# Kernel tuning notes

Measured on AMD Instinct MI355X. Metric: run time of the kernel, lower is better.

The kernel has to match this reference:

```python
import jax, jax.numpy as jnp
import numpy as np

B, S, D = 8, 2048, 512

def setup_inputs() -> dict:
    key = jax.random.key(0)
    k1, k2, k3 = jax.random.split(key, 3)
    context = jax.random.normal(k1, (B, S, D), dtype=jnp.float32)
    # nn.Linear default init ~ U(-1/sqrt(D), 1/sqrt(D)); scale keeps softmax sane
    bound = 1.0 / np.sqrt(D)
    W_in = jax.random.uniform(k2, (D, D), dtype=jnp.float32, minval=-bound, maxval=bound)
    W_out = jax.random.uniform(k3, (D, D), dtype=jnp.float32, minval=-bound, maxval=bound)
    return {"context": context, "W_in": W_in, "W_out": W_out}

def reference(context, W_in, W_out):
    # linear_in: x @ W_in.T (torch Linear convention)
    c = jnp.einsum('bsd,ed->bse', context, W_in)            # [B,S,D]
    scores = jnp.einsum('bsd,btd->bst', c, c)               # [B,S,S], no 1/sqrt(d) scale
    attn = jax.nn.softmax(scores, axis=-1)                  # [B,S,S]
    ctx = jnp.einsum('bst,btd->bsd', attn, c)               # [B,S,D]
    out = jnp.einsum('bsd,ed->bse', jnp.tanh(ctx), W_out)   # linear_out
    return out, attn
```

## Files before the change

kernel.cpp:

```cpp
#include <hip/hip_runtime.h>
#include <cstdint>
#include <cstddef>

#define Bc 8
#define Sc 2048
#define Dc 512

typedef float f32x4 __attribute__((ext_vector_type(4)));
typedef __bf16 bf16x8 __attribute__((ext_vector_type(8)));
typedef __bf16 bf16x4 __attribute__((ext_vector_type(4)));

__device__ __forceinline__ void gload_lds16(const void* g, void* l) {
    __builtin_amdgcn_global_load_lds((const __attribute__((address_space(1))) void*)g,
                                     (__attribute__((address_space(3))) void*)l, 16, 0, 0);
}

__device__ __forceinline__ f32x4 mfma16x16x32(bf16x8 a, bf16x8 b, f32x4 c) {
    return __builtin_amdgcn_mfma_f32_16x16x32_bf16(a, b, c, 0, 0, 0);
}

__global__ void k_convert_w(const float* __restrict__ wi, const float* __restrict__ wo,
                            __bf16* __restrict__ wib, __bf16* __restrict__ wob) {
    int i = blockIdx.x * 256 + threadIdx.x;
    wib[i] = (__bf16)wi[i];
    wob[i] = (__bf16)wo[i];
}

template <bool STATS>
__global__ __launch_bounds__(256) void k_gemm_bf16(
        const __bf16* __restrict__ A, const __bf16* __restrict__ Bt,
        float* __restrict__ C, float2* __restrict__ stats,
        int lda, int ldb, int ldc, int K,
        size_t aOffZ, size_t bOffZ, size_t cOffZ)
{
    __shared__ alignas(16) __bf16 smem[2 * 128 * 64];
    __bf16* As = smem;
    __bf16* Bs = smem + 128 * 64;
    const int tid  = threadIdx.x;
    const int wave = tid >> 6, lane = tid & 63;
    const int waveM = wave >> 1, waveN = wave & 1;
    int row0, col0, bz;
    if constexpr (STATS) {
        const int bid = blockIdx.x;
        bz   = bid & 7;
        col0 = ((bid >> 3) & 15) * 128;
        row0 = (bid >> 7) * 128;
    } else {
        bz = blockIdx.z; row0 = blockIdx.y * 128; col0 = blockIdx.x * 128;
    }
    A  += (size_t)bz * aOffZ;
    Bt += (size_t)bz * bOffZ;
    C  += (size_t)bz * cOffZ;

    f32x4 acc[4][4] = {};

    for (int k0 = 0; k0 < K; k0 += 64) {
        #pragma unroll
        for (int i = 0; i < 4; ++i) {
            int flat = i * 2048 + wave * 512 + lane * 8;
            int r  = flat >> 6;
            int cc = (flat >> 3) & 7;
            int gc = (cc ^ (r & 7)) << 3;
            gload_lds16(A  + (size_t)(row0 + r) * lda + k0 + gc, As + i * 2048 + wave * 512);
            gload_lds16(Bt + (size_t)(col0 + r) * ldb + k0 + gc, Bs + i * 2048 + wave * 512);
        }
        __syncthreads();
        #pragma unroll
        for (int ks = 0; ks < 2; ++ks) {
            const int kc = ks * 4 + (lane >> 4);
            bf16x8 av[4], bv[4];
            #pragma unroll
            for (int mi = 0; mi < 4; ++mi) {
                int r = waveM * 64 + mi * 16 + (lane & 15);
                av[mi] = *(const bf16x8*)&As[r * 64 + ((kc ^ (r & 7)) << 3)];
            }
            #pragma unroll
            for (int ni = 0; ni < 4; ++ni) {
                int r = waveN * 64 + ni * 16 + (lane & 15);
                bv[ni] = *(const bf16x8*)&Bs[r * 64 + ((kc ^ (r & 7)) << 3)];
            }
            #pragma unroll
            for (int mi = 0; mi < 4; ++mi)
                #pragma unroll
                for (int ni = 0; ni < 4; ++ni)
                    acc[mi][ni] = mfma16x16x32(av[mi], bv[ni], acc[mi][ni]);
        }
        __syncthreads();
    }

    const int rb = (lane >> 4) << 2;
    const int cb = lane & 15;
    #pragma unroll
    for (int mi = 0; mi < 4; ++mi)
        #pragma unroll
        for (int ni = 0; ni < 4; ++ni) {
            int gr = row0 + waveM * 64 + mi * 16 + rb;
            int gc = col0 + waveN * 64 + ni * 16 + cb;
            #pragma unroll
            for (int rr = 0; rr < 4; ++rr)
                C[(size_t)(gr + rr) * ldc + gc] = acc[mi][ni][rr];
        }

    if constexpr (STATS) {
        float2* sm = (float2*)smem;
        #pragma unroll
        for (int mi = 0; mi < 4; ++mi)
            #pragma unroll
            for (int rr = 0; rr < 4; ++rr) {
                float mx = fmaxf(fmaxf(acc[mi][0][rr], acc[mi][1][rr]),
                                 fmaxf(acc[mi][2][rr], acc[mi][3][rr]));
                #pragma unroll
                for (int off = 1; off < 16; off <<= 1) mx = fmaxf(mx, __shfl_xor(mx, off));
                float zs = 0.f;
                #pragma unroll
                for (int ni = 0; ni < 4; ++ni) zs += __expf(acc[mi][ni][rr] - mx);
                #pragma unroll
                for (int off = 1; off < 16; off <<= 1) zs += __shfl_xor(zs, off);
                if ((lane & 15) == 0)
                    sm[waveN * 128 + waveM * 64 + mi * 16 + rb + rr] = make_float2(mx, zs);
            }
        __syncthreads();
        if (tid < 128) {
            float2 a2 = sm[tid], b2 = sm[128 + tid];
            float M = fmaxf(a2.x, b2.x);
            float Z = a2.y * __expf(a2.x - M) + b2.y * __expf(b2.x - M);
            stats[((size_t)bz * Sc + row0 + tid) * 16 + (col0 >> 7)] = make_float2(M, Z);
        }
    }
}

__global__ __launch_bounds__(256) void k_stat_combine(const float2* __restrict__ stats,
                                                      float2* __restrict__ rowstat) {
    int r = blockIdx.x * 256 + threadIdx.x;
    float2 s[16];
    #pragma unroll
    for (int i = 0; i < 16; ++i) s[i] = stats[(size_t)r * 16 + i];
    float M = s[0].x;
    #pragma unroll
    for (int i = 1; i < 16; ++i) M = fmaxf(M, s[i].x);
    float Z = 0.f;
    #pragma unroll
    for (int i = 0; i < 16; ++i) Z += s[i].y * __expf(s[i].x - M);
    rowstat[r] = make_float2(M, 1.f / Z);
}

__global__ __launch_bounds__(512) void k_pv_fused(
        float* __restrict__ attn,
        const __bf16* __restrict__ cT,
        const float2* __restrict__ rowstat,
        __bf16* __restrict__ ctx)
{
    __shared__ alignas(16) __bf16 As[2][64 * 32];
    __shared__ alignas(16) __bf16 Bs[2][512 * 32];
    const int tid  = threadIdx.x;
    const int wave = tid >> 6, lane = tid & 63;
    const int b    = blockIdx.x & 7;
    const int row0 = (blockIdx.x >> 3) * 64;
    float* sc = attn + (size_t)b * Sc * Sc;
    const __bf16* Bt = cT + (size_t)b * Dc * Sc;

    const int ar = tid >> 3;
    const int ac = (tid & 7) * 4;
    const float2 st = rowstat[b * Sc + row0 + ar];
    const float m_row = st.x, zinv = st.y;
    const int a_addr = ar * 32 + (((ac >> 3) ^ (ar & 3)) << 3) + (ac & 7);
    float* srow = sc + (size_t)(row0 + ar) * Sc + ac;

    f32x4 acc[4][4] = {};

    auto stageB = [&](int buf, int kt) {
        #pragma unroll
        for (int i = 0; i < 4; ++i) {
            int chunk = i * 512 + wave * 64 + lane;
            int r  = chunk >> 2;
            int cc = chunk & 3;
            gload_lds16(Bt + (size_t)r * Sc + kt + ((cc ^ (r & 3)) << 3),
                        &Bs[buf][(i * 512 + wave * 64) * 8]);
        }
    };

    const int NT = Sc / 32;

    f32x4 s_next = *(const f32x4*)&srow[0];
    f32x4 p;
    #pragma unroll
    for (int j = 0; j < 4; ++j) p[j] = __expf(s_next[j] - m_row) * zinv;
    {
        bf16x4 pb;
        #pragma unroll
        for (int j = 0; j < 4; ++j) pb[j] = (__bf16)p[j];
        *(bf16x4*)&As[0][a_addr] = pb;
    }
    stageB(0, 0);
    s_next = *(const f32x4*)&srow[32];
    __syncthreads();

    for (int t = 0; t < NT; ++t) {
        const int cur = t & 1;
        if (t + 1 < NT) {
            f32x4 pn;
            #pragma unroll
            for (int j = 0; j < 4; ++j) pn[j] = __expf(s_next[j] - m_row) * zinv;
            bf16x4 pb;
            #pragma unroll
            for (int j = 0; j < 4; ++j) pb[j] = (__bf16)pn[j];
            *(bf16x4*)&As[cur ^ 1][a_addr] = pb;
            stageB(cur ^ 1, (t + 1) * 32);
            *(f32x4*)&srow[t * 32] = p;
            if (t + 2 < NT) s_next = *(const f32x4*)&srow[(t + 2) * 32];
            p = pn;
        } else {
            *(f32x4*)&srow[t * 32] = p;
        }
        const int kc = lane >> 4;
        bf16x8 av[4], bv[4];
        #pragma unroll
        for (int mi = 0; mi < 4; ++mi) {
            int r = mi * 16 + (lane & 15);
            av[mi] = *(const bf16x8*)&As[cur][r * 32 + ((kc ^ (r & 3)) << 3)];
        }
        #pragma unroll
        for (int ni = 0; ni < 4; ++ni) {
            int r = wave * 64 + ni * 16 + (lane & 15);
            bv[ni] = *(const bf16x8*)&Bs[cur][r * 32 + ((kc ^ (r & 3)) << 3)];
        }
        #pragma unroll
        for (int mi = 0; mi < 4; ++mi)
            #pragma unroll
            for (int ni = 0; ni < 4; ++ni)
                acc[mi][ni] = mfma16x16x32(av[mi], bv[ni], acc[mi][ni]);
        __syncthreads();
    }

    const int rb = (lane >> 4) << 2;
    const int cb = lane & 15;
    #pragma unroll
    for (int mi = 0; mi < 4; ++mi)
        #pragma unroll
        for (int ni = 0; ni < 4; ++ni) {
            int gr = row0 + mi * 16 + rb;
            int gc = wave * 64 + ni * 16 + cb;
            #pragma unroll
            for (int rr = 0; rr < 4; ++rr)
                ctx[(size_t)(b * Sc + gr + rr) * Dc + gc] = (__bf16)tanhf(acc[mi][ni][rr]);
        }
}

__global__ __launch_bounds__(256) void k_cproj(
        const float* __restrict__ A, const __bf16* __restrict__ Bt,
        __bf16* __restrict__ Cb, __bf16* __restrict__ CTb)
{
    __shared__ alignas(16) char smem[49152];
    float*  Asf = (float*)smem;
    __bf16* Bs  = (__bf16*)(smem + 32768);
    const int tid  = threadIdx.x;
    const int wave = tid >> 6, lane = tid & 63;
    const int waveM = wave >> 1, waveN = wave & 1;
    const int row0 = blockIdx.y * 128;
    const int col0 = blockIdx.x * 128;

    f32x4 acc[4][4] = {};

    for (int k0 = 0; k0 < Dc; k0 += 64) {
        #pragma unroll
        for (int i = 0; i < 8; ++i) {
            int flat = i * 1024 + wave * 256 + lane * 4;
            int r  = flat >> 6;
            int cc = (flat >> 2) & 15;
            int gc = (cc ^ (r & 15)) << 2;
            gload_lds16(A + (size_t)(row0 + r) * Dc + k0 + gc, Asf + i * 1024 + wave * 256);
        }
        #pragma unroll
        for (int i = 0; i < 4; ++i) {
            int flat = i * 2048 + wave * 512 + lane * 8;
            int r  = flat >> 6;
            int cc = (flat >> 3) & 7;
            int gc = (cc ^ (r & 7)) << 3;
            gload_lds16(Bt + (size_t)(col0 + r) * Dc + k0 + gc, Bs + i * 2048 + wave * 512);
        }
        __syncthreads();
        #pragma unroll
        for (int ks = 0; ks < 2; ++ks) {
            const int kc8 = ks * 4 + (lane >> 4);
            const int kc4 = kc8 << 1;
            bf16x8 av[4], bv[4];
            #pragma unroll
            for (int mi = 0; mi < 4; ++mi) {
                int r  = waveM * 64 + mi * 16 + (lane & 15);
                int r4 = r & 15;
                f32x4 lo = *(const f32x4*)&Asf[r * 64 + (((kc4    ) ^ r4) << 2)];
                f32x4 hi = *(const f32x4*)&Asf[r * 64 + (((kc4 + 1) ^ r4) << 2)];
                bf16x8 a;
                a[0] = (__bf16)lo[0]; a[1] = (__bf16)lo[1]; a[2] = (__bf16)lo[2]; a[3] = (__bf16)lo[3];
                a[4] = (__bf16)hi[0]; a[5] = (__bf16)hi[1]; a[6] = (__bf16)hi[2]; a[7] = (__bf16)hi[3];
                av[mi] = a;
            }
            #pragma unroll
            for (int ni = 0; ni < 4; ++ni) {
                int r = waveN * 64 + ni * 16 + (lane & 15);
                bv[ni] = *(const bf16x8*)&Bs[r * 64 + ((kc8 ^ (r & 7)) << 3)];
            }
            #pragma unroll
            for (int mi = 0; mi < 4; ++mi)
                #pragma unroll
                for (int ni = 0; ni < 4; ++ni)
                    acc[mi][ni] = mfma16x16x32(av[mi], bv[ni], acc[mi][ni]);
        }
        __syncthreads();
    }

    const int rb = (lane >> 4) << 2;
    const int cb = lane & 15;
    __bf16* T = (__bf16*)smem;
    #pragma unroll
    for (int mi = 0; mi < 4; ++mi)
        #pragma unroll
        for (int ni = 0; ni < 4; ++ni) {
            int lr = waveM * 64 + mi * 16 + rb;
            int lc = waveN * 64 + ni * 16 + cb;
            #pragma unroll
            for (int rr = 0; rr < 4; ++rr) {
                __bf16 h = (__bf16)acc[mi][ni][rr];
                Cb[(size_t)(row0 + lr + rr) * Dc + col0 + lc] = h;
                T[lc * 136 + lr + rr] = h;
            }
        }
    __syncthreads();
    const int bb = row0 >> 11;
    const int s0 = row0 & 2047;
    #pragma unroll
    for (int i = 0; i < 8; ++i) {
        int n  = i * 16 + (tid >> 4);
        int mo = (tid & 15) * 8;
        bf16x8 v = *(const bf16x8*)&T[n * 136 + mo];
        *(bf16x8*)&CTb[(size_t)bb * Dc * Sc + (size_t)(col0 + n) * Sc + s0 + mo] = v;
    }
}

extern "C" void kernel_launch(void* const* d_in, const int* in_sizes, int n_in,
                              void* d_out, int out_size, void* d_ws, size_t ws_size,
                              hipStream_t stream)
{
    (void)in_sizes; (void)n_in; (void)out_size; (void)ws_size;
    const float* context = (const float*)d_in[0];
    const float* W_in    = (const float*)d_in[1];
    const float* W_out   = (const float*)d_in[2];
    float* out  = (float*)d_out;
    float* attn = out + (size_t)Bc * Sc * Dc;

    char* ws = (char*)d_ws;
    __bf16* c_bf    = (__bf16*)ws;
    __bf16* cT_bf   = (__bf16*)(ws + 16777216);
    __bf16* wi_bf   = (__bf16*)(ws + 33554432);
    __bf16* wo_bf   = (__bf16*)(ws + 34078720);
    float2* stats   = (float2*)(ws + 34603008);
    float2* rowstat = (float2*)(ws + 36700160);

    k_convert_w<<<dim3(Dc * Dc / 256), 256, 0, stream>>>(W_in, W_out, wi_bf, wo_bf);

    k_cproj<<<dim3(Dc / 128, (Bc * Sc) / 128), 256, 0, stream>>>(context, wi_bf, c_bf, cT_bf);

    k_gemm_bf16<true><<<dim3(Bc * 16 * 16), 256, 0, stream>>>(
        c_bf, c_bf, attn, stats, Dc, Dc, Sc, Dc,
        (size_t)Sc * Dc, (size_t)Sc * Dc, (size_t)Sc * Sc);

    k_stat_combine<<<dim3(Bc * Sc / 256), 256, 0, stream>>>(stats, rowstat);

    k_pv_fused<<<dim3((Sc / 64) * Bc), 512, 0, stream>>>(attn, cT_bf, rowstat, c_bf);

    k_gemm_bf16<false><<<dim3(Dc / 128, (Bc * Sc) / 128, 1), 256, 0, stream>>>(
        c_bf, wo_bf, out, nullptr, Dc, Dc, Dc, Dc, 0, 0, 0);
}
```

Before: 201.3 us.

## Load B operand directly from global in PV kernel, single-buffer A with 64-wide K

```diff
diff --git a/kernel.cpp b/kernel.cpp
--- a/kernel.cpp
+++ b/kernel.cpp
@@ -150,8 +150,7 @@
         const float2* __restrict__ rowstat,
         __bf16* __restrict__ ctx)
 {
-    __shared__ alignas(16) __bf16 As[2][64 * 32];
-    __shared__ alignas(16) __bf16 Bs[2][512 * 32];
+    __shared__ alignas(16) __bf16 As[64 * 64];
     const int tid  = threadIdx.x;
     const int wave = tid >> 6, lane = tid & 63;
     const int b    = blockIdx.x & 7;
@@ -160,76 +159,88 @@
     const __bf16* Bt = cT + (size_t)b * Dc * Sc;
 
     const int ar = tid >> 3;
-    const int ac = (tid & 7) * 4;
+    const int ac = (tid & 7) * 8;
     const float2 st = rowstat[b * Sc + row0 + ar];
     const float m_row = st.x, zinv = st.y;
-    const int a_addr = ar * 32 + (((ac >> 3) ^ (ar & 3)) << 3) + (ac & 7);
+    const int a_addr = ar * 64 + ((((ac >> 3)) ^ (ar & 7)) << 3);
     float* srow = sc + (size_t)(row0 + ar) * Sc + ac;
 
+    const __bf16* bbase[4];
+    #pragma unroll
+    for (int ni = 0; ni < 4; ++ni)
+        bbase[ni] = Bt + (size_t)(wave * 64 + ni * 16 + (lane & 15)) * Sc + (lane >> 4) * 8;
+
     f32x4 acc[4][4] = {};
 
-    auto stageB = [&](int buf, int kt) {
-        #pragma unroll
-        for (int i = 0; i < 4; ++i) {
-            int chunk = i * 512 + wave * 64 + lane;
-            int r  = chunk >> 2;
-            int cc = chunk & 3;
-            gload_lds16(Bt + (size_t)r * Sc + kt + ((cc ^ (r & 3)) << 3),
-                        &Bs[buf][(i * 512 + wave * 64) * 8]);
-        }
-    };
-
-    const int NT = Sc / 32;
-
-    f32x4 s_next = *(const f32x4*)&srow[0];
-    f32x4 p;
-    #pragma unroll
-    for (int j = 0; j < 4; ++j) p[j] = __expf(s_next[j] - m_row) * zinv;
+    const int NT = Sc / 64;
+
+    f32x4 sn0 = *(const f32x4*)&srow[0];
+    f32x4 sn1 = *(const f32x4*)&srow[4];
     {
-        bf16x4 pb;
-        #pragma unroll
-        for (int j = 0; j < 4; ++j) pb[j] = (__bf16)p[j];
-        *(bf16x4*)&As[0][a_addr] = pb;
-    }
-    stageB(0, 0);
-    s_next = *(const f32x4*)&srow[32];
-    __syncthreads();
+        f32x4 p0, p1;
+        #pragma unroll
+        for (int j = 0; j < 4; ++j) {
+            p0[j] = __expf(sn0[j] - m_row) * zinv;
+            p1[j] = __expf(sn1[j] - m_row) * zinv;
+        }
+        bf16x8 pb;
+        #pragma unroll
+        for (int j = 0; j < 4; ++j) { pb[j] = (__bf16)p0[j]; pb[4 + j] = (__bf16)p1[j]; }
+        *(bf16x8*)&As[a_addr] = pb;
+        *(f32x4*)&srow[0] = p0;
+        *(f32x4*)&srow[4] = p1;
+    }
+    asm volatile("s_waitcnt lgkmcnt(0)" ::: "memory");
+    __builtin_amdgcn_s_barrier();
+    sn0 = *(const f32x4*)&srow[64];
+    sn1 = *(const f32x4*)&srow[68];
 
     for (int t = 0; t < NT; ++t) {
-        const int cur = t & 1;
+        bf16x8 av[4][2];
+        #pragma unroll
+        for (int ks = 0; ks < 2; ++ks) {
+            const int kc = ks * 4 + (lane >> 4);
+            #pragma unroll
+            for (int mi = 0; mi < 4; ++mi) {
+                int r = mi * 16 + (lane & 15);
+                av[mi][ks] = *(const bf16x8*)&As[r * 64 + ((kc ^ (r & 7)) << 3)];
+            }
+        }
+        __builtin_amdgcn_s_barrier();
         if (t + 1 < NT) {
-            f32x4 pn;
-            #pragma unroll
-            for (int j = 0; j < 4; ++j) pn[j] = __expf(s_next[j] - m_row) * zinv;
-            bf16x4 pb;
-            #pragma unroll
-            for (int j = 0; j < 4; ++j) pb[j] = (__bf16)pn[j];
-            *(bf16x4*)&As[cur ^ 1][a_addr] = pb;
-            stageB(cur ^ 1, (t + 1) * 32);
-            *(f32x4*)&srow[t * 32] = p;
-            if (t + 2 < NT) s_next = *(const f32x4*)&srow[(t + 2) * 32];
-            p = pn;
-        } else {
-            *(f32x4*)&srow[t * 32] = p;
-        }
-        const int kc = lane >> 4;
-        bf16x8 av[4], bv[4];
-        #pragma unroll
-        for (int mi = 0; mi < 4; ++mi) {
-            int r = mi * 16 + (lane & 15);
-            av[mi] = *(const bf16x8*)&As[cur][r * 32 + ((kc ^ (r & 3)) << 3)];
-        }
-        #pragma unroll
-        for (int ni = 0; ni < 4; ++ni) {
-            int r = wave * 64 + ni * 16 + (lane & 15);
-            bv[ni] = *(const bf16x8*)&Bs[cur][r * 32 + ((kc ^ (r & 3)) << 3)];
-        }
-        #pragma unroll
-        for (int mi = 0; mi < 4; ++mi)
+            f32x4 p0, p1;
+            #pragma unroll
+            for (int j = 0; j < 4; ++j) {
+                p0[j] = __expf(sn0[j] - m_row) * zinv;
+                p1[j] = __expf(sn1[j] - m_row) * zinv;
+            }
+            bf16x8 pb;
+            #pragma unroll
+            for (int j = 0; j < 4; ++j) { pb[j] = (__bf16)p0[j]; pb[4 + j] = (__bf16)p1[j]; }
+            *(bf16x8*)&As[a_addr] = pb;
+            *(f32x4*)&srow[(t + 1) * 64]     = p0;
+            *(f32x4*)&srow[(t + 1) * 64 + 4] = p1;
+            if (t + 2 < NT) {
+                sn0 = *(const f32x4*)&srow[(t + 2) * 64];
+                sn1 = *(const f32x4*)&srow[(t + 2) * 64 + 4];
+            }
+        }
+        const int kt = t * 64;
+        bf16x8 bv[2][4];
+        #pragma unroll
+        for (int ks = 0; ks < 2; ++ks)
             #pragma unroll
             for (int ni = 0; ni < 4; ++ni)
-                acc[mi][ni] = mfma16x16x32(av[mi], bv[ni], acc[mi][ni]);
-        __syncthreads();
+                bv[ks][ni] = *(const bf16x8*)(bbase[ni] + kt + ks * 32);
+        #pragma unroll
+        for (int ks = 0; ks < 2; ++ks)
+            #pragma unroll
+            for (int mi = 0; mi < 4; ++mi)
+                #pragma unroll
+                for (int ni = 0; ni < 4; ++ni)
+                    acc[mi][ni] = mfma16x16x32(av[mi][ks], bv[ks][ni], acc[mi][ni]);
+        asm volatile("s_waitcnt lgkmcnt(0)" ::: "memory");
+        __builtin_amdgcn_s_barrier();
     }
 
     const int rb = (lane >> 4) << 2;
```

After: 213.3 us. 1.06x slower.
